# Kernel optimization log

Hardware: AMD Instinct MI355X
Metric: run time of the kernel (lower is better)

## Reference

```python
import jax, jax.numpy as jnp
import numpy as np

B, T, V, H, W = 2, 4, 4, 128, 128
NQ = 64
QDIM, IDIM, MDIM = 256, 32, 16

def setup_inputs() -> dict:
    key = jax.random.key(0)
    ks = jax.random.split(key, 9)
    return {
        "instance_affinity": jax.random.normal(ks[0], (B, T, V, H, W, IDIM), dtype=jnp.float32),
        "motion_code": jax.random.normal(ks[1], (B, T, V, H, W, MDIM), dtype=jnp.float32),
        "query_feat": jax.random.normal(ks[2], (B, T, NQ, QDIM), dtype=jnp.float32),
        "assignment_prob": jax.random.uniform(ks[3], (B, T, V, H, W, NQ + 1), dtype=jnp.float32),
        "assigned_query": jax.random.randint(ks[4], (B, T, V, H, W), 0, NQ + 1, dtype=jnp.int64),
        "W_inst": jax.random.normal(ks[5], (QDIM, IDIM), dtype=jnp.float32) * 0.02,
        "b_inst": jax.random.normal(ks[6], (IDIM,), dtype=jnp.float32) * 0.02,
        "W_motion": jax.random.normal(ks[7], (QDIM, MDIM), dtype=jnp.float32) * 0.02,
        "b_motion": jax.random.normal(ks[8], (MDIM,), dtype=jnp.float32) * 0.02,
    }

def reference(instance_affinity, motion_code, query_feat, assignment_prob, assigned_query, W_inst, b_inst, W_motion, b_motion):
    # project queries: (b,t,q,query_dim) -> (b,t,q,d)
    query_inst = query_feat @ W_inst + b_inst      # (b,t,q,32)
    query_motion = query_feat @ W_motion + b_motion  # (b,t,q,16)
    bg_prob = assignment_prob[..., :1]   # (b,t,v,h,w,1)
    fg_prob = assignment_prob[..., 1:]   # (b,t,v,h,w,nq)
    fg_norm = jnp.maximum(fg_prob.sum(axis=-1, keepdims=True), 1e-6)
    # weighted-sum pooling over queries as a fused contraction (no huge broadcast intermediate)
    pooled_inst = jnp.einsum('btvhwq,btqd->btvhwd', fg_prob, query_inst) / fg_norm
    pooled_motion = jnp.einsum('btvhwq,btqd->btvhwd', fg_prob, query_motion) / fg_norm
    refine_gate = 1.0 - bg_prob
    inst = instance_affinity + refine_gate * pooled_inst
    motion = motion_code + refine_gate * pooled_motion
    entity_id = assigned_query  # already (b,t,v,h,w)
    return (entity_id, inst, motion)
```

## Files before the change

kernel.cpp:

```cpp
#include <hip/hip_runtime.h>

#define BT     8
#define VHW    (4*128*128)
#define NQn    64
#define QD     256
#define ID     32
#define MD     16
#define CD     48
#define APW    65
#define LOCS   128
#define PPITCH 52

typedef short bf16x8 __attribute__((ext_vector_type(8)));
typedef float f32x4  __attribute__((ext_vector_type(4)));

static __device__ __forceinline__ short f2bf(float f) {
    unsigned u = __builtin_bit_cast(unsigned, f);
    unsigned r = (u + 0x7FFFu + ((u >> 16) & 1u)) >> 16;
    return (short)r;
}

__global__ __launch_bounds__(256) void qproj_kernel(
    const float* __restrict__ qf,
    const float* __restrict__ Wi,
    const float* __restrict__ bi,
    const float* __restrict__ Wm,
    const float* __restrict__ bm,
    short* __restrict__ qtabB)
{
    int idx = blockIdx.x * 256 + threadIdx.x;
    int btq = idx / CD;
    int d   = idx - btq * CD;
    int bt  = btq >> 6;
    int q   = btq & 63;
    const float* __restrict__ qrow = qf + btq * QD;
    float a;
    if (d < ID) {
        a = bi[d];
        #pragma unroll 8
        for (int k = 0; k < QD; ++k) a = fmaf(qrow[k], Wi[k*ID + d], a);
    } else {
        int dm = d - ID;
        a = bm[dm];
        #pragma unroll 8
        for (int k = 0; k < QD; ++k) a = fmaf(qrow[k], Wm[k*MD + dm], a);
    }
    int nt = d >> 4, c = d & 15;
    int kt = q >> 5, kk = q & 31;
    int lane = ((kk >> 3) << 4) | c;
    int j    = kk & 7;
    qtabB[((((bt*3 + nt)*2 + kt) << 6) + lane) * 8 + j] = f2bf(a);
}

__global__ __launch_bounds__(256, 4) void entity_kernel(
    const float* __restrict__ ia,
    const float* __restrict__ mc,
    const float* __restrict__ ap,
    const int*   __restrict__ aq,
    const short* __restrict__ qtabB,
    float* __restrict__ out_id,
    float* __restrict__ out_inst,
    float* __restrict__ out_mot)
{
    __shared__ __align__(16) float smem[LOCS * APW];
    __shared__ float psum_s[LOCS];
    __shared__ float scale_s[LOCS];

    const int  t    = threadIdx.x;
    const int  lane = t & 63;
    const int  w    = t >> 6;
    const int  bt   = blockIdx.x >> 9;
    const long base = (long)blockIdx.x * LOCS;

    {
        const float4* __restrict__ src = (const float4*)(ap + base * APW);
        float4* __restrict__ dst = (float4*)smem;
        #pragma unroll
        for (int k = 0; k < 8; ++k) dst[t + 256 * k] = src[t + 256 * k];
        if (t < (LOCS * APW / 4 - 2048)) dst[2048 + t] = src[2048 + t];
    }

    bf16x8 Bf[3][2];
    {
        const bf16x8* __restrict__ qb = (const bf16x8*)(qtabB + bt * (3*2*64*8));
        #pragma unroll
        for (int nt = 0; nt < 3; ++nt)
            #pragma unroll
            for (int kt = 0; kt < 2; ++kt)
                Bf[nt][kt] = qb[(nt*2 + kt) * 64 + lane];
    }
    bf16x8 Bones;
    {
        short one = ((lane & 15) == 0) ? (short)0x3F80 : (short)0;
        #pragma unroll
        for (int j = 0; j < 8; ++j) Bones[j] = one;
    }

    float4 ia_r[4], mc_r[2];
    float  idv = 0.f;
    {
        const float4* __restrict__ ia4 = (const float4*)(ia + base * ID);
        const float4* __restrict__ mc4 = (const float4*)(mc + base * MD);
        #pragma unroll
        for (int k = 0; k < 4; ++k) ia_r[k] = ia4[t + 256 * k];
        #pragma unroll
        for (int k = 0; k < 2; ++k) mc_r[k] = mc4[t + 256 * k];
        if (t < LOCS) idv = (float)aq[base + t];
    }

    __syncthreads();

    const int c = lane & 15, g = lane >> 4;
    f32x4 acc[2][3];
    f32x4 accP[2];
    #pragma unroll
    for (int m = 0; m < 2; ++m) {
        accP[m] = (f32x4){0.f, 0.f, 0.f, 0.f};
        #pragma unroll
        for (int n = 0; n < 3; ++n) acc[m][n] = (f32x4){0.f, 0.f, 0.f, 0.f};
    }
    #pragma unroll
    for (int kt = 0; kt < 2; ++kt) {
        #pragma unroll
        for (int m = 0; m < 2; ++m) {
            const float* __restrict__ ar = smem + (w*32 + m*16 + c) * APW + 1 + kt*32 + g*8;
            bf16x8 A;
            #pragma unroll
            for (int j = 0; j < 8; ++j) A[j] = f2bf(ar[j]);
            acc[m][0] = __builtin_amdgcn_mfma_f32_16x16x32_bf16(A, Bf[0][kt], acc[m][0], 0, 0, 0);
            acc[m][1] = __builtin_amdgcn_mfma_f32_16x16x32_bf16(A, Bf[1][kt], acc[m][1], 0, 0, 0);
            acc[m][2] = __builtin_amdgcn_mfma_f32_16x16x32_bf16(A, Bf[2][kt], acc[m][2], 0, 0, 0);
            accP[m]   = __builtin_amdgcn_mfma_f32_16x16x32_bf16(A, Bones,     accP[m],   0, 0, 0);
        }
    }

    if (c == 0) {
        #pragma unroll
        for (int m = 0; m < 2; ++m)
            #pragma unroll
            for (int r = 0; r < 4; ++r)
                psum_s[w*32 + m*16 + g*4 + r] = accP[m][r];
    }
    __syncthreads();
    if (t < LOCS)
        scale_s[t] = (1.0f - smem[t * APW]) / fmaxf(psum_s[t], 1e-6f);
    __syncthreads();

    #pragma unroll
    for (int m = 0; m < 2; ++m) {
        const int lrow = w*32 + m*16 + g*4;
        #pragma unroll
        for (int r = 0; r < 4; ++r) {
            const float s  = scale_s[lrow + r];
            const int   po = (lrow + r) * PPITCH;
            smem[po + c]      = s * acc[m][0][r];
            smem[po + 16 + c] = s * acc[m][1][r];
            smem[po + 32 + c] = s * acc[m][2][r];
        }
    }
    __syncthreads();

    float4* __restrict__ oi4 = (float4*)(out_inst + base * ID);
    float4* __restrict__ om4 = (float4*)(out_mot  + base * MD);
    #pragma unroll
    for (int k = 0; k < 4; ++k) {
        int i = t + 256 * k;
        int loc = i >> 3, d4 = i & 7;
        const float* p = smem + loc * PPITCH + d4 * 4;
        float4 v = ia_r[k];
        v.x += p[0]; v.y += p[1]; v.z += p[2]; v.w += p[3];
        oi4[i] = v;
    }
    #pragma unroll
    for (int k = 0; k < 2; ++k) {
        int i = t + 256 * k;
        int loc = i >> 2, d4 = i & 3;
        const float* p = smem + loc * PPITCH + 32 + d4 * 4;
        float4 v = mc_r[k];
        v.x += p[0]; v.y += p[1]; v.z += p[2]; v.w += p[3];
        om4[i] = v;
    }
    if (t < LOCS) out_id[base + t] = idv;
}

extern "C" void kernel_launch(void* const* d_in, const int* in_sizes, int n_in,
                              void* d_out, int out_size, void* d_ws, size_t ws_size,
                              hipStream_t stream) {
    const float* ia = (const float*)d_in[0];
    const float* mc = (const float*)d_in[1];
    const float* qf = (const float*)d_in[2];
    const float* ap = (const float*)d_in[3];
    const int*   aq = (const int*)  d_in[4];
    const float* Wi = (const float*)d_in[5];
    const float* bi = (const float*)d_in[6];
    const float* Wm = (const float*)d_in[7];
    const float* bm = (const float*)d_in[8];

    short* qtabB = (short*)d_ws;

    float* out_id   = (float*)d_out;
    float* out_inst = out_id + (long)BT * VHW;
    float* out_mot  = out_inst + (long)BT * VHW * ID;

    qproj_kernel<<<(BT * NQn * CD) / 256, 256, 0, stream>>>(qf, Wi, bi, Wm, bm, qtabB);
    entity_kernel<<<(BT * VHW) / LOCS, 256, 0, stream>>>(ia, mc, ap, aq, qtabB,
                                                         out_id, out_inst, out_mot);
}
```

Baseline: 329.8 us.

## Load MFMA operands directly from global, drop LDS staging and barriers

```diff
diff --git a/kernel.cpp b/kernel.cpp
--- a/kernel.cpp
+++ b/kernel.cpp
@@ -8,8 +8,6 @@
 #define MD     16
 #define CD     48
 #define APW    65
-#define LOCS   128
-#define PPITCH 52
 
 typedef short bf16x8 __attribute__((ext_vector_type(8)));
 typedef float f32x4  __attribute__((ext_vector_type(4)));
@@ -28,31 +26,39 @@
     const float* __restrict__ bm,
     short* __restrict__ qtabB)
 {
-    int idx = blockIdx.x * 256 + threadIdx.x;
-    int btq = idx / CD;
-    int d   = idx - btq * CD;
-    int bt  = btq >> 6;
-    int q   = btq & 63;
-    const float* __restrict__ qrow = qf + btq * QD;
-    float a;
-    if (d < ID) {
-        a = bi[d];
-        #pragma unroll 8
-        for (int k = 0; k < QD; ++k) a = fmaf(qrow[k], Wi[k*ID + d], a);
-    } else {
-        int dm = d - ID;
-        a = bm[dm];
-        #pragma unroll 8
-        for (int k = 0; k < QD; ++k) a = fmaf(qrow[k], Wm[k*MD + dm], a);
+    __shared__ float part[4][CD];
+    const int btq = blockIdx.x;
+    const int bt  = btq >> 6;
+    const int q   = btq & 63;
+    const int ks  = threadIdx.x >> 6;
+    const int d   = threadIdx.x & 63;
+
+    if (d < CD) {
+        const float* __restrict__ qrow = qf + btq * QD + ks * 64;
+        float a = 0.f;
+        if (d < ID) {
+            #pragma unroll 8
+            for (int j = 0; j < 64; ++j) a = fmaf(qrow[j], Wi[(ks*64 + j)*ID + d], a);
+        } else {
+            const int dm = d - ID;
+            #pragma unroll 8
+            for (int j = 0; j < 64; ++j) a = fmaf(qrow[j], Wm[(ks*64 + j)*MD + dm], a);
+        }
+        part[ks][d] = a;
     }
-    int nt = d >> 4, c = d & 15;
-    int kt = q >> 5, kk = q & 31;
-    int lane = ((kk >> 3) << 4) | c;
-    int j    = kk & 7;
-    qtabB[((((bt*3 + nt)*2 + kt) << 6) + lane) * 8 + j] = f2bf(a);
+    __syncthreads();
+    if (ks == 0 && d < CD) {
+        float s = (d < ID ? bi[d] : bm[d - ID])
+                + part[0][d] + part[1][d] + part[2][d] + part[3][d];
+        const int nt = d >> 4, c = d & 15;
+        const int kt = q >> 5, kk = q & 31;
+        const int lane = ((kk >> 3) << 4) | c;
+        const int j    = kk & 7;
+        qtabB[((((bt*3 + nt)*2 + kt) << 6) + lane) * 8 + j] = f2bf(s);
+    }
 }
 
-__global__ __launch_bounds__(256, 4) void entity_kernel(
+__global__ __launch_bounds__(256) void entity_kernel(
     const float* __restrict__ ia,
     const float* __restrict__ mc,
     const float* __restrict__ ap,
@@ -62,23 +68,13 @@
     float* __restrict__ out_inst,
     float* __restrict__ out_mot)
 {
-    __shared__ __align__(16) float smem[LOCS * APW];
-    __shared__ float psum_s[LOCS];
-    __shared__ float scale_s[LOCS];
-
-    const int  t    = threadIdx.x;
-    const int  lane = t & 63;
-    const int  w    = t >> 6;
-    const int  bt   = blockIdx.x >> 9;
-    const long base = (long)blockIdx.x * LOCS;
-
-    {
-        const float4* __restrict__ src = (const float4*)(ap + base * APW);
-        float4* __restrict__ dst = (float4*)smem;
-        #pragma unroll
-        for (int k = 0; k < 8; ++k) dst[t + 256 * k] = src[t + 256 * k];
-        if (t < (LOCS * APW / 4 - 2048)) dst[2048 + t] = src[2048 + t];
-    }
+    const int t    = threadIdx.x;
+    const int lane = t & 63;
+    const int w    = t >> 6;
+    const int c    = lane & 15;
+    const int g    = lane >> 4;
+    const int bt   = blockIdx.x >> 9;
+    const long rb  = (long)blockIdx.x * 128 + w * 32;
 
     bf16x8 Bf[3][2];
     {
@@ -89,98 +85,82 @@
             for (int kt = 0; kt < 2; ++kt)
                 Bf[nt][kt] = qb[(nt*2 + kt) * 64 + lane];
     }
-    bf16x8 Bones;
-    {
-        short one = ((lane & 15) == 0) ? (short)0x3F80 : (short)0;
-        #pragma unroll
-        for (int j = 0; j < 8; ++j) Bones[j] = one;
-    }
 
-    float4 ia_r[4], mc_r[2];
-    float  idv = 0.f;
-    {
-        const float4* __restrict__ ia4 = (const float4*)(ia + base * ID);
-        const float4* __restrict__ mc4 = (const float4*)(mc + base * MD);
-        #pragma unroll
-        for (int k = 0; k < 4; ++k) ia_r[k] = ia4[t + 256 * k];
-        #pragma unroll
-        for (int k = 0; k < 2; ++k) mc_r[k] = mc4[t + 256 * k];
-        if (t < LOCS) idv = (float)aq[base + t];
-    }
-
-    __syncthreads();
-
-    const int c = lane & 15, g = lane >> 4;
-    f32x4 acc[2][3];
-    f32x4 accP[2];
+    float Af[2][2][8];
+    float bg[2];
     #pragma unroll
     for (int m = 0; m < 2; ++m) {
-        accP[m] = (f32x4){0.f, 0.f, 0.f, 0.f};
+        const float* __restrict__ arow = ap + (rb + m*16 + c) * APW;
+        bg[m] = arow[0];
         #pragma unroll
-        for (int n = 0; n < 3; ++n) acc[m][n] = (f32x4){0.f, 0.f, 0.f, 0.f};
-    }
-    #pragma unroll
-    for (int kt = 0; kt < 2; ++kt) {
-        #pragma unroll
-        for (int m = 0; m < 2; ++m) {
-            const float* __restrict__ ar = smem + (w*32 + m*16 + c) * APW + 1 + kt*32 + g*8;
-            bf16x8 A;
+        for (int kt = 0; kt < 2; ++kt) {
+            const float* __restrict__ ar = arow + 1 + kt*32 + g*8;
             #pragma unroll
-            for (int j = 0; j < 8; ++j) A[j] = f2bf(ar[j]);
-            acc[m][0] = __builtin_amdgcn_mfma_f32_16x16x32_bf16(A, Bf[0][kt], acc[m][0], 0, 0, 0);
-            acc[m][1] = __builtin_amdgcn_mfma_f32_16x16x32_bf16(A, Bf[1][kt], acc[m][1], 0, 0, 0);
-            acc[m][2] = __builtin_amdgcn_mfma_f32_16x16x32_bf16(A, Bf[2][kt], acc[m][2], 0, 0, 0);
-            accP[m]   = __builtin_amdgcn_mfma_f32_16x16x32_bf16(A, Bones,     accP[m],   0, 0, 0);
+            for (int j = 0; j < 8; ++j) Af[m][kt][j] = ar[j];
         }
     }
 
-    if (c == 0) {
+    float ia_r[2][2][4], mc_r[2][4];
+    #pragma unroll
+    for (int m = 0; m < 2; ++m)
         #pragma unroll
-        for (int m = 0; m < 2; ++m)
+        for (int r = 0; r < 4; ++r) {
+            const long row = rb + m*16 + 4*g + r;
+            ia_r[m][0][r] = ia[row*ID + c];
+            ia_r[m][1][r] = ia[row*ID + 16 + c];
+            mc_r[m][r]    = mc[row*MD + c];
+        }
+    float idv = 0.f;
+    if (lane < 32) idv = (float)aq[rb + lane];
+
+    float scale[2][4];
+    #pragma unroll
+    for (int m = 0; m < 2; ++m) {
+        float s = 0.f;
+        #pragma unroll
+        for (int kt = 0; kt < 2; ++kt)
             #pragma unroll
-            for (int r = 0; r < 4; ++r)
-                psum_s[w*32 + m*16 + g*4 + r] = accP[m][r];
+            for (int j = 0; j < 8; ++j) s += Af[m][kt][j];
+        s += __shfl_xor(s, 16);
+        s += __shfl_xor(s, 32);
+        const float sc = (1.0f - bg[m]) / fmaxf(s, 1e-6f);
+        #pragma unroll
+        for (int r = 0; r < 4; ++r) scale[m][r] = __shfl(sc, 4*g + r);
     }
-    __syncthreads();
-    if (t < LOCS)
-        scale_s[t] = (1.0f - smem[t * APW]) / fmaxf(psum_s[t], 1e-6f);
-    __syncthreads();
+
+    bf16x8 Ab[2][2];
+    #pragma unroll
+    for (int m = 0; m < 2; ++m)
+        #pragma unroll
+        for (int kt = 0; kt < 2; ++kt)
+            #pragma unroll
+            for (int j = 0; j < 8; ++j) Ab[m][kt][j] = f2bf(Af[m][kt][j]);
+
+    f32x4 acc[2][3];
+    #pragma unroll
+    for (int m = 0; m < 2; ++m)
+        #pragma unroll
+        for (int n = 0; n < 3; ++n) acc[m][n] = (f32x4){0.f, 0.f, 0.f, 0.f};
+    #pragma unroll
+    for (int kt = 0; kt < 2; ++kt)
+        #pragma unroll
+        for (int m = 0; m < 2; ++m) {
+            acc[m][0] = __builtin_amdgcn_mfma_f32_16x16x32_bf16(Ab[m][kt], Bf[0][kt], acc[m][0], 0, 0, 0);
+            acc[m][1] = __builtin_amdgcn_mfma_f32_16x16x32_bf16(Ab[m][kt], Bf[1][kt], acc[m][1], 0, 0, 0);
+            acc[m][2] = __builtin_amdgcn_mfma_f32_16x16x32_bf16(Ab[m][kt], Bf[2][kt], acc[m][2], 0, 0, 0);
+        }
 
     #pragma unroll
-    for (int m = 0; m < 2; ++m) {
-        const int lrow = w*32 + m*16 + g*4;
+    for (int m = 0; m < 2; ++m)
         #pragma unroll
         for (int r = 0; r < 4; ++r) {
-            const float s  = scale_s[lrow + r];
-            const int   po = (lrow + r) * PPITCH;
-            smem[po + c]      = s * acc[m][0][r];
-            smem[po + 16 + c] = s * acc[m][1][r];
-            smem[po + 32 + c] = s * acc[m][2][r];
+            const long row = rb + m*16 + 4*g + r;
+            const float s = scale[m][r];
+            out_inst[row*ID + c]      = ia_r[m][0][r] + s * acc[m][0][r];
+            out_inst[row*ID + 16 + c] = ia_r[m][1][r] + s * acc[m][1][r];
+            out_mot [row*MD + c]      = mc_r[m][r]    + s * acc[m][2][r];
         }
-    }
-    __syncthreads();
-
-    float4* __restrict__ oi4 = (float4*)(out_inst + base * ID);
-    float4* __restrict__ om4 = (float4*)(out_mot  + base * MD);
-    #pragma unroll
-    for (int k = 0; k < 4; ++k) {
-        int i = t + 256 * k;
-        int loc = i >> 3, d4 = i & 7;
-        const float* p = smem + loc * PPITCH + d4 * 4;
-        float4 v = ia_r[k];
-        v.x += p[0]; v.y += p[1]; v.z += p[2]; v.w += p[3];
-        oi4[i] = v;
-    }
-    #pragma unroll
-    for (int k = 0; k < 2; ++k) {
-        int i = t + 256 * k;
-        int loc = i >> 2, d4 = i & 3;
-        const float* p = smem + loc * PPITCH + 32 + d4 * 4;
-        float4 v = mc_r[k];
-        v.x += p[0]; v.y += p[1]; v.z += p[2]; v.w += p[3];
-        om4[i] = v;
-    }
-    if (t < LOCS) out_id[base + t] = idv;
+    if (lane < 32) out_id[rb + lane] = idv;
 }
 
 extern "C" void kernel_launch(void* const* d_in, const int* in_sizes, int n_in,
@@ -202,7 +182,7 @@
     float* out_inst = out_id + (long)BT * VHW;
     float* out_mot  = out_inst + (long)BT * VHW * ID;
 
-    qproj_kernel<<<(BT * NQn * CD) / 256, 256, 0, stream>>>(qf, Wi, bi, Wm, bm, qtabB);
-    entity_kernel<<<(BT * VHW) / LOCS, 256, 0, stream>>>(ia, mc, ap, aq, qtabB,
-                                                         out_id, out_inst, out_mot);
+    qproj_kernel<<<BT * NQn, 256, 0, stream>>>(qf, Wi, bi, Wm, bm, qtabB);
+    entity_kernel<<<(BT * VHW) / 128, 256, 0, stream>>>(ia, mc, ap, aq, qtabB,
+                                                        out_id, out_inst, out_mot);
 }
```

Result: faster. 311.1 us (-5.7%).
